# Performance work log

Hardware: AMD Instinct MI355X
Metric: run time of the kernel (lower is better)

## Reference

```python
import jax, jax.numpy as jnp
import numpy as np

B = 524288        # batch of configurations
NJ = 8            # chain joints (7 revolute + 1 fixed)
NA = 7            # active (revolute) joints


def setup_inputs() -> dict:
    key = jax.random.key(0)
    k1, k2, k3 = jax.random.split(key, 3)
    joint_positions = jax.random.normal(k1, (B, NA), dtype=jnp.float32)
    # fixed origin transforms: random 3x4 top block, homogeneous bottom row
    top = jax.random.normal(k2, (NJ, 3, 4), dtype=jnp.float32)
    bottom = jnp.tile(jnp.array([[[0.0, 0.0, 0.0, 1.0]]], dtype=jnp.float32), (NJ, 1, 1))
    fixed_transforms = jnp.concatenate([top, bottom], axis=1)  # [NJ,4,4]
    axes = jax.random.normal(k3, (NA, 3), dtype=jnp.float32)
    joint_axes = axes / jnp.linalg.norm(axes, axis=-1, keepdims=True)  # unit axes
    return {"joint_positions": joint_positions,
            "fixed_transforms": fixed_transforms,
            "joint_axes": joint_axes}


def _skew(axes):
    # axes: [NA,3] -> K: [NA,3,3]
    x, y, z = axes[:, 0], axes[:, 1], axes[:, 2]
    o = jnp.zeros_like(x)
    return jnp.stack([
        jnp.stack([o, -z, y], axis=-1),
        jnp.stack([z, o, -x], axis=-1),
        jnp.stack([-y, x, o], axis=-1),
    ], axis=-2)


def reference(joint_positions, fixed_transforms, joint_axes):
    b = joint_positions.shape[0]
    dtype = joint_positions.dtype
    K = _skew(joint_axes)                      # [NA,3,3]
    KK = jnp.einsum('jab,jbc->jac', K, K)      # [NA,3,3]
    theta = joint_positions[:, :, None, None]  # [B,NA,1,1]
    I3 = jnp.eye(3, dtype=dtype)
    # Rodrigues: R = I + sin(t) K + (1 - cos(t)) K^2, all joints at once
    R = I3 + jnp.sin(theta) * K + (1.0 - jnp.cos(theta)) * KK  # [B,NA,3,3]
    joint_tf = jnp.zeros((b, NA, 4, 4), dtype=dtype)
    joint_tf = joint_tf.at[:, :, :3, :3].set(R).at[:, :, 3, 3].set(1.0)
    # per-joint total transform: fixed origin @ joint motion
    M_active = jnp.einsum('jab,njbc->njac', fixed_transforms[:NA], joint_tf)  # [B,NA,4,4]
    M_last = jnp.broadcast_to(fixed_transforms[NA], (b, 1, 4, 4))             # fixed joint
    M = jnp.concatenate([M_active, M_last], axis=1)                           # [B,NJ,4,4]
    # sequential chain accumulation: T <- T @ M_i
    T0 = jnp.broadcast_to(jnp.eye(4, dtype=dtype), (b, 4, 4))
    def step(T, Mi):
        return jnp.einsum('nab,nbc->nac', T, Mi), None
    T, _ = jax.lax.scan(step, T0, jnp.moveaxis(M, 1, 0))
    return T
```

## Files before the change

kernel.cpp:

```cpp
#include <hip/hip_runtime.h>

#define NA 7
#define BLK 256

__global__ __launch_bounds__(BLK) void fk_kernel(
    const float* __restrict__ jp,
    const float* __restrict__ ft,
    const float* __restrict__ ax,
    float* __restrict__ out)
{
    __shared__ float cst[7 * 30 + 12];
    __shared__ float lin[BLK * 7];
    __shared__ float lout[BLK * 16];

    const int t = threadIdx.x;
    const long long blockBase = (long long)blockIdx.x * BLK;

    const float* jpb = jp + blockBase * 7;
    #pragma unroll
    for (int k = 0; k < 7; ++k)
        lin[t + k * BLK] = jpb[t + k * BLK];

    if (t < 8) {
        const int j = t;
        const float* F = ft + j * 16;
        float F3[9] = {F[0], F[1], F[2], F[4], F[5], F[6], F[8], F[9], F[10]};
        float tv[3] = {F[3], F[7], F[11]};
        if (j < NA) {
            float x = ax[j * 3 + 0], y = ax[j * 3 + 1], z = ax[j * 3 + 2];
            float K[9] = {0.f, -z, y,  z, 0.f, -x,  -y, x, 0.f};
            float KK[9];
            for (int a = 0; a < 3; ++a)
                for (int c = 0; c < 3; ++c) {
                    float s = 0.f;
                    for (int b = 0; b < 3; ++b) s += K[a * 3 + b] * K[b * 3 + c];
                    KK[a * 3 + c] = s;
                }
            float* dst = cst + j * 30;
            for (int i = 0; i < 9; ++i) dst[i] = F3[i];
            for (int a = 0; a < 3; ++a)
                for (int c = 0; c < 3; ++c) {
                    float q = 0.f, s2 = 0.f;
                    for (int b = 0; b < 3; ++b) {
                        q  += F3[a * 3 + b] * K[b * 3 + c];
                        s2 += F3[a * 3 + b] * KK[b * 3 + c];
                    }
                    dst[9 + a * 3 + c]  = q;
                    dst[18 + a * 3 + c] = s2;
                }
            dst[27] = tv[0]; dst[28] = tv[1]; dst[29] = tv[2];
        } else {
            float* dst = cst + 210;
            for (int i = 0; i < 9; ++i) dst[i] = F3[i];
            dst[9] = tv[0]; dst[10] = tv[1]; dst[11] = tv[2];
        }
    }
    __syncthreads();

    float sv[NA], cv[NA];
    #pragma unroll
    for (int j = 0; j < NA; ++j) {
        float th = lin[t * 7 + j];
        __sincosf(th, &sv[j], &cv[j]);
    }

    float A[9], tr[3];
    {
        const float* d = cst;
        float sj = sv[0], oc = 1.0f - cv[0];
        #pragma unroll
        for (int i = 0; i < 9; ++i) A[i] = d[i] + sj * d[9 + i] + oc * d[18 + i];
        tr[0] = d[27]; tr[1] = d[28]; tr[2] = d[29];
    }
    #pragma unroll
    for (int j = 1; j < NA; ++j) {
        const float* d = cst + j * 30;
        float sj = sv[j], oc = 1.0f - cv[j];
        float m[9];
        #pragma unroll
        for (int i = 0; i < 9; ++i) m[i] = d[i] + sj * d[9 + i] + oc * d[18 + i];
        float t0 = tr[0] + A[0] * d[27] + A[1] * d[28] + A[2] * d[29];
        float t1 = tr[1] + A[3] * d[27] + A[4] * d[28] + A[5] * d[29];
        float t2 = tr[2] + A[6] * d[27] + A[7] * d[28] + A[8] * d[29];
        tr[0] = t0; tr[1] = t1; tr[2] = t2;
        float N[9];
        #pragma unroll
        for (int a = 0; a < 3; ++a)
            #pragma unroll
            for (int c = 0; c < 3; ++c)
                N[a * 3 + c] = A[a * 3 + 0] * m[c] + A[a * 3 + 1] * m[3 + c] + A[a * 3 + 2] * m[6 + c];
        #pragma unroll
        for (int i = 0; i < 9; ++i) A[i] = N[i];
    }
    {
        const float* d = cst + 210;
        float t0 = tr[0] + A[0] * d[9] + A[1] * d[10] + A[2] * d[11];
        float t1 = tr[1] + A[3] * d[9] + A[4] * d[10] + A[5] * d[11];
        float t2 = tr[2] + A[6] * d[9] + A[7] * d[10] + A[8] * d[11];
        tr[0] = t0; tr[1] = t1; tr[2] = t2;
        float N[9];
        #pragma unroll
        for (int a = 0; a < 3; ++a)
            #pragma unroll
            for (int c = 0; c < 3; ++c)
                N[a * 3 + c] = A[a * 3 + 0] * d[c] + A[a * 3 + 1] * d[3 + c] + A[a * 3 + 2] * d[6 + c];
        #pragma unroll
        for (int i = 0; i < 9; ++i) A[i] = N[i];
    }

    float* o = lout + t * 16;
    o[0]  = A[0]; o[1]  = A[1]; o[2]  = A[2]; o[3]  = tr[0];
    o[4]  = A[3]; o[5]  = A[4]; o[6]  = A[5]; o[7]  = tr[1];
    o[8]  = A[6]; o[9]  = A[7]; o[10] = A[8]; o[11] = tr[2];
    o[12] = 0.f;  o[13] = 0.f;  o[14] = 0.f;  o[15] = 1.f;
    __syncthreads();

    const float4* l4 = (const float4*)lout;
    float4* o4 = (float4*)out + blockBase * 4;
    #pragma unroll
    for (int k = 0; k < 4; ++k)
        o4[t + k * BLK] = l4[t + k * BLK];
}

extern "C" void kernel_launch(void* const* d_in, const int* in_sizes, int n_in,
                              void* d_out, int out_size, void* d_ws, size_t ws_size,
                              hipStream_t stream) {
    const float* jp = (const float*)d_in[0];
    const float* ft = (const float*)d_in[1];
    const float* ax = (const float*)d_in[2];
    float* out = (float*)d_out;
    const int B = in_sizes[0] / 7;
    fk_kernel<<<dim3(B / BLK), dim3(BLK), 0, stream>>>(jp, ft, ax, out);
}
```

Before: 85.29 us.

## Precompute joint constants in a prep kernel and stage data per wave without barriers

Moves the per-joint constant setup (skew, K^2, fixed-transform products) into a separate single-block prep kernel that writes to workspace, so the main kernel reads the constants from global memory. The main kernel stages inputs and outputs through a per-wavefront shared buffer using float4 loads and stores, with XOR swizzling to avoid LDS bank conflicts. Block-wide __syncthreads are replaced with lgkmcnt waits, and sincos is computed inline. This removes barrier stalls and the serial 8-thread constant computation from every block, at the cost of an extra kernel launch and relying on wave-local synchronisation being sufficient.

```diff
diff --git a/kernel.cpp b/kernel.cpp
--- a/kernel.cpp
+++ b/kernel.cpp
@@ -3,82 +3,94 @@
 #define NA 7
 #define BLK 256
 
+__global__ void prep_kernel(const float* __restrict__ ft,
+                            const float* __restrict__ ax,
+                            float* __restrict__ cst)
+{
+    const int j = threadIdx.x;
+    if (j >= 8) return;
+    const float* F = ft + j * 16;
+    float F3[9] = {F[0], F[1], F[2], F[4], F[5], F[6], F[8], F[9], F[10]};
+    float tv[3] = {F[3], F[7], F[11]};
+    if (j < NA) {
+        float x = ax[j * 3 + 0], y = ax[j * 3 + 1], z = ax[j * 3 + 2];
+        float K[9] = {0.f, -z, y,  z, 0.f, -x,  -y, x, 0.f};
+        float KK[9];
+        #pragma unroll
+        for (int a = 0; a < 3; ++a)
+            #pragma unroll
+            for (int c = 0; c < 3; ++c) {
+                float s = 0.f;
+                #pragma unroll
+                for (int b = 0; b < 3; ++b) s += K[a * 3 + b] * K[b * 3 + c];
+                KK[a * 3 + c] = s;
+            }
+        float* dst = cst + j * 30;
+        #pragma unroll
+        for (int i = 0; i < 9; ++i) dst[i] = F3[i];
+        #pragma unroll
+        for (int a = 0; a < 3; ++a)
+            #pragma unroll
+            for (int c = 0; c < 3; ++c) {
+                float q = 0.f, s2 = 0.f;
+                #pragma unroll
+                for (int b = 0; b < 3; ++b) {
+                    q  += F3[a * 3 + b] * K[b * 3 + c];
+                    s2 += F3[a * 3 + b] * KK[b * 3 + c];
+                }
+                dst[9  + a * 3 + c] = q;
+                dst[18 + a * 3 + c] = s2;
+            }
+        dst[27] = tv[0]; dst[28] = tv[1]; dst[29] = tv[2];
+    } else {
+        float* dst = cst + 210;
+        #pragma unroll
+        for (int i = 0; i < 9; ++i) dst[i] = F3[i];
+        dst[9] = tv[0]; dst[10] = tv[1]; dst[11] = tv[2];
+    }
+}
+
 __global__ __launch_bounds__(BLK) void fk_kernel(
     const float* __restrict__ jp,
-    const float* __restrict__ ft,
-    const float* __restrict__ ax,
+    const float* __restrict__ cst,
     float* __restrict__ out)
 {
-    __shared__ float cst[7 * 30 + 12];
-    __shared__ float lin[BLK * 7];
-    __shared__ float lout[BLK * 16];
+    __shared__ __attribute__((aligned(16))) float buf[BLK * 16];
 
     const int t = threadIdx.x;
-    const long long blockBase = (long long)blockIdx.x * BLK;
+    const int l = t & 63;
+    const int w = t >> 6;
+    const long long waveItem = (long long)blockIdx.x * BLK + (w << 6);
 
-    const float* jpb = jp + blockBase * 7;
-    #pragma unroll
-    for (int k = 0; k < 7; ++k)
-        lin[t + k * BLK] = jpb[t + k * BLK];
+    float* wbuf = buf + (w << 10);
 
-    if (t < 8) {
-        const int j = t;
-        const float* F = ft + j * 16;
-        float F3[9] = {F[0], F[1], F[2], F[4], F[5], F[6], F[8], F[9], F[10]};
-        float tv[3] = {F[3], F[7], F[11]};
-        if (j < NA) {
-            float x = ax[j * 3 + 0], y = ax[j * 3 + 1], z = ax[j * 3 + 2];
-            float K[9] = {0.f, -z, y,  z, 0.f, -x,  -y, x, 0.f};
-            float KK[9];
-            for (int a = 0; a < 3; ++a)
-                for (int c = 0; c < 3; ++c) {
-                    float s = 0.f;
-                    for (int b = 0; b < 3; ++b) s += K[a * 3 + b] * K[b * 3 + c];
-                    KK[a * 3 + c] = s;
-                }
-            float* dst = cst + j * 30;
-            for (int i = 0; i < 9; ++i) dst[i] = F3[i];
-            for (int a = 0; a < 3; ++a)
-                for (int c = 0; c < 3; ++c) {
-                    float q = 0.f, s2 = 0.f;
-                    for (int b = 0; b < 3; ++b) {
-                        q  += F3[a * 3 + b] * K[b * 3 + c];
-                        s2 += F3[a * 3 + b] * KK[b * 3 + c];
-                    }
-                    dst[9 + a * 3 + c]  = q;
-                    dst[18 + a * 3 + c] = s2;
-                }
-            dst[27] = tv[0]; dst[28] = tv[1]; dst[29] = tv[2];
-        } else {
-            float* dst = cst + 210;
-            for (int i = 0; i < 9; ++i) dst[i] = F3[i];
-            dst[9] = tv[0]; dst[10] = tv[1]; dst[11] = tv[2];
-        }
+    {
+        const float4* g4 = (const float4*)(jp + waveItem * 7);
+        float4* s4 = (float4*)wbuf;
+        s4[l] = g4[l];
+        if (l < 48) s4[64 + l] = g4[64 + l];
     }
-    __syncthreads();
-
-    float sv[NA], cv[NA];
-    #pragma unroll
-    for (int j = 0; j < NA; ++j) {
-        float th = lin[t * 7 + j];
-        __sincosf(th, &sv[j], &cv[j]);
-    }
+    asm volatile("s_waitcnt lgkmcnt(0)" ::: "memory");
 
     float A[9], tr[3];
     {
+        float s, c;
+        __sincosf(wbuf[l * 7 + 0], &s, &c);
+        const float oc = 1.0f - c;
         const float* d = cst;
-        float sj = sv[0], oc = 1.0f - cv[0];
         #pragma unroll
-        for (int i = 0; i < 9; ++i) A[i] = d[i] + sj * d[9 + i] + oc * d[18 + i];
+        for (int i = 0; i < 9; ++i) A[i] = d[i] + s * d[9 + i] + oc * d[18 + i];
         tr[0] = d[27]; tr[1] = d[28]; tr[2] = d[29];
     }
     #pragma unroll
     for (int j = 1; j < NA; ++j) {
         const float* d = cst + j * 30;
-        float sj = sv[j], oc = 1.0f - cv[j];
+        float s, c;
+        __sincosf(wbuf[l * 7 + j], &s, &c);
+        const float oc = 1.0f - c;
         float m[9];
         #pragma unroll
-        for (int i = 0; i < 9; ++i) m[i] = d[i] + sj * d[9 + i] + oc * d[18 + i];
+        for (int i = 0; i < 9; ++i) m[i] = d[i] + s * d[9 + i] + oc * d[18 + i];
         float t0 = tr[0] + A[0] * d[27] + A[1] * d[28] + A[2] * d[29];
         float t1 = tr[1] + A[3] * d[27] + A[4] * d[28] + A[5] * d[29];
         float t2 = tr[2] + A[6] * d[27] + A[7] * d[28] + A[8] * d[29];
@@ -87,8 +99,8 @@
         #pragma unroll
         for (int a = 0; a < 3; ++a)
             #pragma unroll
-            for (int c = 0; c < 3; ++c)
-                N[a * 3 + c] = A[a * 3 + 0] * m[c] + A[a * 3 + 1] * m[3 + c] + A[a * 3 + 2] * m[6 + c];
+            for (int c2 = 0; c2 < 3; ++c2)
+                N[a * 3 + c2] = A[a * 3 + 0] * m[c2] + A[a * 3 + 1] * m[3 + c2] + A[a * 3 + 2] * m[6 + c2];
         #pragma unroll
         for (int i = 0; i < 9; ++i) A[i] = N[i];
     }
@@ -102,24 +114,30 @@
         #pragma unroll
         for (int a = 0; a < 3; ++a)
             #pragma unroll
-            for (int c = 0; c < 3; ++c)
-                N[a * 3 + c] = A[a * 3 + 0] * d[c] + A[a * 3 + 1] * d[3 + c] + A[a * 3 + 2] * d[6 + c];
+            for (int c2 = 0; c2 < 3; ++c2)
+                N[a * 3 + c2] = A[a * 3 + 0] * d[c2] + A[a * 3 + 1] * d[3 + c2] + A[a * 3 + 2] * d[6 + c2];
         #pragma unroll
         for (int i = 0; i < 9; ++i) A[i] = N[i];
     }
 
-    float* o = lout + t * 16;
-    o[0]  = A[0]; o[1]  = A[1]; o[2]  = A[2]; o[3]  = tr[0];
-    o[4]  = A[3]; o[5]  = A[4]; o[6]  = A[5]; o[7]  = tr[1];
-    o[8]  = A[6]; o[9]  = A[7]; o[10] = A[8]; o[11] = tr[2];
-    o[12] = 0.f;  o[13] = 0.f;  o[14] = 0.f;  o[15] = 1.f;
-    __syncthreads();
-
-    const float4* l4 = (const float4*)lout;
-    float4* o4 = (float4*)out + blockBase * 4;
-    #pragma unroll
-    for (int k = 0; k < 4; ++k)
-        o4[t + k * BLK] = l4[t + k * BLK];
+    float4* wb4 = (float4*)wbuf;
+    {
+        const int x = (l >> 1) & 7;
+        wb4[(4 * l + 0) ^ x] = make_float4(A[0], A[1], A[2], tr[0]);
+        wb4[(4 * l + 1) ^ x] = make_float4(A[3], A[4], A[5], tr[1]);
+        wb4[(4 * l + 2) ^ x] = make_float4(A[6], A[7], A[8], tr[2]);
+        wb4[(4 * l + 3) ^ x] = make_float4(0.f, 0.f, 0.f, 1.f);
+    }
+    asm volatile("s_waitcnt lgkmcnt(0)" ::: "memory");
+    {
+        float4* o4 = (float4*)out + waveItem * 4;
+        const int y = (l >> 3) & 7;
+        #pragma unroll
+        for (int k = 0; k < 4; ++k) {
+            const int s = l + (k << 6);
+            o4[s] = wb4[s ^ y];
+        }
+    }
 }
 
 extern "C" void kernel_launch(void* const* d_in, const int* in_sizes, int n_in,
@@ -129,6 +147,8 @@
     const float* ft = (const float*)d_in[1];
     const float* ax = (const float*)d_in[2];
     float* out = (float*)d_out;
+    float* cst = (float*)d_ws;
     const int B = in_sizes[0] / 7;
-    fk_kernel<<<dim3(B / BLK), dim3(BLK), 0, stream>>>(jp, ft, ax, out);
+    prep_kernel<<<dim3(1), dim3(64), 0, stream>>>(ft, ax, cst);
+    fk_kernel<<<dim3(B / BLK), dim3(BLK), 0, stream>>>(jp, cst, out);
 }
```

Measured after the change: 81.43 us. -4.5%, faster.
